# Kernel tuning notes

Measured on AMD Instinct MI355X. Metric: run time of the kernel, lower is better.

The kernel has to match this reference:

```python
import jax, jax.numpy as jnp
import numpy as np

EMBED_DIM = 1024

def setup_inputs() -> dict:
    key = jax.random.key(0)
    k1, k2 = jax.random.split(key)
    x = jax.random.normal(k1, (8, 2048, EMBED_DIM), dtype=jnp.float32)
    # torch nn.Linear weight is [out, in]; emulate default init scale roughly
    W_qkv = jax.random.normal(k2, (3 * EMBED_DIM, EMBED_DIM), dtype=jnp.float32) * (1.0 / np.sqrt(EMBED_DIM))
    b_qkv = jnp.zeros((3 * EMBED_DIM,), dtype=jnp.float32)
    return {"x": x, "W_qkv": W_qkv, "b_qkv": b_qkv}

def reference(x, W_qkv, b_qkv):
    # qkv = x @ W.T + b  -> [B, N, 3E]
    qkv = jnp.einsum('bne,fe->bnf', x, W_qkv) + b_qkv
    q, k, v = jnp.split(qkv, 3, axis=-1)  # each [B, N, E]
    scale = 1.0 / jnp.sqrt(jnp.asarray(EMBED_DIM, dtype=x.dtype))
    scores = jnp.einsum('bqe,bke->bqk', q, k) * scale  # [B, N, N]
    attn = jax.nn.softmax(scores, axis=-1)
    return jnp.einsum('bqk,bke->bqe', attn, v)
```

## Files before the change

kernel.cpp:

```cpp
#include <hip/hip_runtime.h>
#include <hip/hip_bf16.h>

typedef unsigned short u16;
typedef unsigned int   u32;
typedef long long      ll;

#define BATCH   8
#define SEQ     2048
#define EMBED   1024
#define THREE_E 3072

using bf16x8 = __attribute__((ext_vector_type(8))) __bf16;
using f32x4  = __attribute__((ext_vector_type(4))) float;

typedef const __attribute__((address_space(1))) void* as1cv;
typedef __attribute__((address_space(3))) void*       as3v;

__device__ __forceinline__ float bf2f(u16 u) {
  union { float f; u32 i; } c; c.i = ((u32)u) << 16; return c.f;
}
__device__ __forceinline__ u16 f2bf(float f) {
  u32 u = __builtin_bit_cast(u32, f);
  return (u16)((u + 0x7FFFu + ((u >> 16) & 1u)) >> 16);
}

__global__ __launch_bounds__(256) void cast_f32_bf16(const float* __restrict__ in,
                                                     u16* __restrict__ out, int n4) {
  int i = blockIdx.x * 256 + threadIdx.x;
  int stride = gridDim.x * 256;
  for (; i < n4; i += stride) {
    float4 f = ((const float4*)in)[i];
    ushort4 o;
    o.x = f2bf(f.x); o.y = f2bf(f.y); o.z = f2bf(f.z); o.w = f2bf(f.w);
    ((ushort4*)out)[i] = o;
  }
}

template<int STORE_BF16, int HAS_BIAS>
__global__ __launch_bounds__(512) void gemm256(
    const u16* __restrict__ A, const u16* __restrict__ B,
    void* __restrict__ Cv, const float* __restrict__ bias,
    int lda, int ldb, int ldc, int nt, float scale,
    ll sA, ll sB, ll sC, int gx, int gy)
{
  __shared__ __align__(128) char smem[131072];
  const int tid = threadIdx.x;
  const int w  = tid >> 6, l = tid & 63;
  const int lr  = l & 15;
  const int lkb = (l >> 4) * 16;
  const int wm  = w >> 2, wn = w & 3;

  const int nwg = gridDim.x;
  const int id  = blockIdx.x;
  const int sid = (id & 7) * (nwg >> 3) + (id >> 3);
  const int bx  = sid % gx;
  const int tq  = sid / gx;
  const int by  = tq % gy;
  const int bz  = tq / gy;
  const ll  tileM = (ll)by * 256;
  const int tileN = bx * 256;
  A += (ll)bz * sA;
  B += (ll)bz * sB;

  const int rh0  = tid >> 3;
  const int cbyt = ((tid & 7) * 16) ^ ((rh0 & 7) << 4);
  const int kofs = cbyt >> 1;
  const u16* Asrc = A + (tileM + rh0) * lda + kofs;
  const u16* Bsrc = B + ((ll)tileN + (rh0 >> 5) * 64 + (rh0 & 31)) * ldb + kofs;
  char* lwb = smem + w * 1024;

#define STAGE_A(D,H,KT) do{ \
  const u16* g_ = Asrc + (ll)(H)*64*lda + (KT)*64; \
  char* lb_ = lwb + (D)*65536 + (H)*16384; \
  __builtin_amdgcn_global_load_lds((as1cv)g_, (as3v)lb_, 16, 0, 0); \
  __builtin_amdgcn_global_load_lds((as1cv)(g_ + 128LL*lda), (as3v)(lb_ + 8192), 16, 0, 0); \
}while(0)

#define STAGE_B(D,H,KT) do{ \
  const u16* g_ = Bsrc + (ll)(H)*32*ldb + (KT)*64; \
  char* lb_ = lwb + (D)*65536 + 32768 + (H)*16384; \
  __builtin_amdgcn_global_load_lds((as1cv)g_, (as3v)lb_, 16, 0, 0); \
  __builtin_amdgcn_global_load_lds((as1cv)(g_ + 128LL*ldb), (as3v)(lb_ + 8192), 16, 0, 0); \
}while(0)

  bf16x8 a_[4][2], b0_[2][2], b1_[2][2];
  f32x4 acc[8][4] = {};

#define LDA8(D,MH) do{ \
  _Pragma("unroll") for (int mi = 0; mi < 4; ++mi) { \
    const int rh_ = wm*64 + mi*16 + lr; \
    const char* rp_ = smem + (D)*65536 + (MH)*16384 + rh_*128; \
    const int sw_ = (rh_ & 7) << 4; \
    a_[mi][0] = *(const bf16x8*)(rp_ + (lkb ^ sw_)); \
    a_[mi][1] = *(const bf16x8*)(rp_ + ((64 + lkb) ^ sw_)); \
  } \
}while(0)

#define LDB4(BB,D,NH) do{ \
  _Pragma("unroll") for (int ni = 0; ni < 2; ++ni) { \
    const int rh_ = wn*32 + ni*16 + lr; \
    const char* rp_ = smem + (D)*65536 + 32768 + (NH)*16384 + rh_*128; \
    const int sw_ = (rh_ & 7) << 4; \
    BB[ni][0] = *(const bf16x8*)(rp_ + (lkb ^ sw_)); \
    BB[ni][1] = *(const bf16x8*)(rp_ + ((64 + lkb) ^ sw_)); \
  } \
}while(0)

#define MFMA16(MH,NH,BB) do{ \
  __builtin_amdgcn_s_setprio(1); \
  _Pragma("unroll") for (int ks = 0; ks < 2; ++ks) \
    _Pragma("unroll") for (int mi = 0; mi < 4; ++mi) \
      _Pragma("unroll") for (int ni = 0; ni < 2; ++ni) \
        acc[(MH)*4+mi][(NH)*2+ni] = __builtin_amdgcn_mfma_f32_16x16x32_bf16( \
            a_[mi][ks], BB[ni][ks], acc[(MH)*4+mi][(NH)*2+ni], 0, 0, 0); \
  __builtin_amdgcn_s_setprio(0); \
}while(0)

#define BAR() __builtin_amdgcn_s_barrier()
#define WAIT_LGKM0() do{ asm volatile("s_waitcnt lgkmcnt(0)":::"memory"); \
                         __builtin_amdgcn_sched_barrier(0); }while(0)

  STAGE_A(0,0,0); STAGE_B(0,0,0); STAGE_A(0,1,0); STAGE_B(0,1,0);
  STAGE_A(1,0,1); STAGE_B(1,1,1);
  asm volatile("s_waitcnt vmcnt(4)":::"memory");
  BAR();

  const int NI = nt >> 1;
  for (int it = 0; it < NI; ++it) {
    const int k1 = 2*it + 1, k2 = 2*it + 2, k3 = 2*it + 3;
    const bool pf = (it + 1 < NI);
    LDA8(0,0); LDB4(b0_,0,0);
    STAGE_A(1,1,k1);
    asm volatile("s_waitcnt lgkmcnt(8)":::"memory");
    BAR(); WAIT_LGKM0();
    MFMA16(0,0,b0_);
    BAR();
    LDB4(b1_,0,1);
    STAGE_B(1,0,k1);
    BAR(); WAIT_LGKM0();
    MFMA16(0,1,b1_);
    BAR();
    LDA8(0,1);
    if (pf) STAGE_A(0,0,k2);
    BAR(); WAIT_LGKM0();
    MFMA16(1,1,b1_);
    BAR();
    LDB4(b0_,0,0);
    if (pf) STAGE_B(0,1,k2);
    BAR(); WAIT_LGKM0();
    MFMA16(1,0,b0_);
    if (pf) asm volatile("s_waitcnt vmcnt(4)":::"memory");
    else    asm volatile("s_waitcnt vmcnt(0)":::"memory");
    BAR();
    LDA8(1,0); LDB4(b0_,1,0);
    if (pf) STAGE_A(0,1,k2);
    asm volatile("s_waitcnt lgkmcnt(8)":::"memory");
    BAR(); WAIT_LGKM0();
    MFMA16(0,0,b0_);
    BAR();
    LDB4(b1_,1,1);
    if (pf) STAGE_B(0,0,k2);
    BAR(); WAIT_LGKM0();
    MFMA16(0,1,b1_);
    BAR();
    LDA8(1,1);
    if (pf) STAGE_A(1,0,k3);
    BAR(); WAIT_LGKM0();
    MFMA16(1,1,b1_);
    BAR();
    LDB4(b0_,1,0);
    if (pf) STAGE_B(1,1,k3);
    BAR(); WAIT_LGKM0();
    MFMA16(1,0,b0_);
    if (pf) asm volatile("s_waitcnt vmcnt(4)":::"memory");
    else    asm volatile("s_waitcnt vmcnt(0)":::"memory");
    BAR();
  }

  u16*   Cb = (u16*)Cv   + (ll)bz * sC;
  float* Cf = (float*)Cv + (ll)bz * sC;
  const ll rbase = tileM + wm * 128 + (l >> 4) * 4;
#pragma unroll
  for (int m = 0; m < 8; ++m) {
    const ll row0 = rbase + (m >> 2) * 64 + (m & 3) * 16;
#pragma unroll
    for (int n = 0; n < 4; ++n) {
      const int col = tileN + wn * 64 + n * 16 + lr;
      float badd = HAS_BIAS ? bias[col] : 0.0f;
#pragma unroll
      for (int j = 0; j < 4; ++j) {
        float v = acc[m][n][j] * scale + badd;
        if (STORE_BF16) Cb[(row0 + j) * ldc + col] = f2bf(v);
        else            Cf[(row0 + j) * ldc + col] = v;
      }
    }
  }
#undef STAGE_A
#undef STAGE_B
#undef LDA8
#undef LDB4
#undef MFMA16
#undef BAR
#undef WAIT_LGKM0
}

__global__ __launch_bounds__(256) void transpose_v(const u16* __restrict__ qkv,
                                                   u16* __restrict__ Vt) {
  __shared__ u16 tile[64 * 64];
  const int t  = threadIdx.x;
  const int b  = blockIdx.z;
  const int e0 = blockIdx.x * 64;
  const int n0 = blockIdx.y * 64;
  const u16* V  = qkv + (ll)b * SEQ * THREE_E + 2 * EMBED;
  u16* Vtb      = Vt  + (ll)b * EMBED * SEQ;
  const int r = t >> 3;
  const int c = (t & 7) * 8;
#pragma unroll
  for (int p = 0; p < 2; ++p) {
    const int rr = r + p * 32;
    uint4 d = *(const uint4*)&V[(ll)(n0 + rr) * THREE_E + e0 + c];
    *(uint4*)&tile[rr * 64 + (c ^ ((rr & 7) << 3))] = d;
  }
  __syncthreads();
#pragma unroll
  for (int p = 0; p < 2; ++p) {
    const int er = r + p * 32;
    u16 o[8];
#pragma unroll
    for (int i = 0; i < 8; ++i) {
      const int nn = c + i;
      o[i] = tile[nn * 64 + (er ^ ((nn & 7) << 3))];
    }
    *(uint4*)&Vtb[(ll)(e0 + er) * SEQ + n0 + c] = *(const uint4*)o;
  }
}

__global__ __launch_bounds__(256) void softmax_rows(u16* __restrict__ S) {
  const ll row = blockIdx.x;
  u16* p = S + row * SEQ;
  const int t = threadIdx.x;
  uint4 raw = ((const uint4*)p)[t];
  const u16* rs = (const u16*)&raw;
  float v[8];
#pragma unroll
  for (int i = 0; i < 8; ++i) v[i] = bf2f(rs[i]);
  float m = v[0];
#pragma unroll
  for (int i = 1; i < 8; ++i) m = fmaxf(m, v[i]);
#pragma unroll
  for (int off = 32; off > 0; off >>= 1) m = fmaxf(m, __shfl_xor(m, off));
  __shared__ float red[8];
  if ((t & 63) == 0) red[t >> 6] = m;
  __syncthreads();
  m = fmaxf(fmaxf(red[0], red[1]), fmaxf(red[2], red[3]));
  float e[8];
  float s = 0.0f;
#pragma unroll
  for (int i = 0; i < 8; ++i) { e[i] = __expf(v[i] - m); s += e[i]; }
#pragma unroll
  for (int off = 32; off > 0; off >>= 1) s += __shfl_xor(s, off);
  if ((t & 63) == 0) red[4 + (t >> 6)] = s;
  __syncthreads();
  s = red[4] + red[5] + red[6] + red[7];
  const float inv = 1.0f / s;
  u16 o[8];
#pragma unroll
  for (int i = 0; i < 8; ++i) o[i] = f2bf(e[i] * inv);
  ((uint4*)p)[t] = *(const uint4*)o;
}

extern "C" void kernel_launch(void* const* d_in, const int* in_sizes, int n_in,
                              void* d_out, int out_size, void* d_ws, size_t ws_size,
                              hipStream_t stream) {
  const float* x    = (const float*)d_in[0];
  const float* W    = (const float*)d_in[1];
  const float* bias = (const float*)d_in[2];
  float* out = (float*)d_out;
  char* ws = (char*)d_ws;
  (void)in_sizes; (void)n_in; (void)out_size; (void)ws_size;

  u16* qkv = (u16*)ws;
  u16* Sbf = (u16*)(ws + 100663296LL);
  u16* Vt  = (u16*)(ws + 100663296LL + 67108864LL);
  u16* xb  = (u16*)(ws + 100663296LL);
  u16* Wb  = (u16*)(ws + 100663296LL + 33554432LL);

  cast_f32_bf16<<<dim3(2048), dim3(256), 0, stream>>>(x, xb, (BATCH*SEQ*EMBED) / 4);
  cast_f32_bf16<<<dim3(512),  dim3(256), 0, stream>>>(W, Wb, (THREE_E*EMBED) / 4);

  gemm256<1, 1><<<dim3(768), dim3(512), 0, stream>>>(
      xb, Wb, (void*)qkv, bias, EMBED, EMBED, THREE_E, EMBED/64, 1.0f,
      0LL, 0LL, 0LL, 12, 64);

  transpose_v<<<dim3(EMBED/64, SEQ/64, BATCH), dim3(256), 0, stream>>>(qkv, Vt);

  gemm256<1, 0><<<dim3(512), dim3(512), 0, stream>>>(
      qkv, qkv + EMBED, (void*)Sbf, (const float*)nullptr,
      THREE_E, THREE_E, SEQ, EMBED/64, 0.03125f,
      (ll)SEQ * THREE_E, (ll)SEQ * THREE_E, (ll)SEQ * SEQ, 8, 8);

  softmax_rows<<<dim3(BATCH * SEQ), dim3(256), 0, stream>>>(Sbf);

  gemm256<0, 0><<<dim3(256), dim3(512), 0, stream>>>(
      Sbf, Vt, (void*)out, (const float*)nullptr,
      SEQ, SEQ, EMBED, SEQ/64, 1.0f,
      (ll)SEQ * SEQ, (ll)EMBED * SEQ, (ll)SEQ * EMBED, 4, 8);
}
```

Baseline: 388.0 us.

## Restructure GEMM main loop into eight-phase ping-pong with deeper prefetch

Rewrites the bf16 GEMM inner loop as eight uniform phases. Each phase waits on a single combined vmcnt/lgkmcnt barrier, then reads the next LDS fragment, issues a global-to-LDS stage, and runs MFMAs on fragments loaded in the previous phase. It double-buffers the A and B register fragments so LDS reads overlap the MFMAs, and hoists the swizzled LDS pointer math out of the loop. Out-of-range tiles are clamped so loads issue unconditionally rather than behind branches. This adds register pressure and redundant loads near the end of the loop, in exchange for deeper global-load queuing (vmcnt 12).

```diff
diff --git a/kernel.cpp b/kernel.cpp
--- a/kernel.cpp
+++ b/kernel.cpp
@@ -83,98 +83,84 @@
   __builtin_amdgcn_global_load_lds((as1cv)(g_ + 128LL*ldb), (as3v)(lb_ + 8192), 16, 0, 0); \
 }while(0)
 
-  bf16x8 a_[4][2], b0_[2][2], b1_[2][2];
+  const int sw  = (lr & 7) << 4;
+  const int ok0 = lkb ^ sw;
+  const int ok1 = (64 + lkb) ^ sw;
+  const char* pA0k0 = smem + (wm * 64 + lr) * 128 + ok0;
+  const char* pA0k1 = smem + (wm * 64 + lr) * 128 + ok1;
+  const char* pA1k0 = pA0k0 + 65536;
+  const char* pA1k1 = pA0k1 + 65536;
+  const char* pB0k0 = smem + 32768 + (wn * 32 + lr) * 128 + ok0;
+  const char* pB0k1 = smem + 32768 + (wn * 32 + lr) * 128 + ok1;
+  const char* pB1k0 = pB0k0 + 65536;
+  const char* pB1k1 = pB0k1 + 65536;
+
+  bf16x8 aA[4][2], aB[4][2], bX[2][2], bY[2][2];
   f32x4 acc[8][4] = {};
 
-#define LDA8(D,MH) do{ \
+#define READ_A(DST, PK0, PK1, MH) do{ \
   _Pragma("unroll") for (int mi = 0; mi < 4; ++mi) { \
-    const int rh_ = wm*64 + mi*16 + lr; \
-    const char* rp_ = smem + (D)*65536 + (MH)*16384 + rh_*128; \
-    const int sw_ = (rh_ & 7) << 4; \
-    a_[mi][0] = *(const bf16x8*)(rp_ + (lkb ^ sw_)); \
-    a_[mi][1] = *(const bf16x8*)(rp_ + ((64 + lkb) ^ sw_)); \
+    DST[mi][0] = *(const bf16x8*)((PK0) + (MH)*16384 + mi*2048); \
+    DST[mi][1] = *(const bf16x8*)((PK1) + (MH)*16384 + mi*2048); \
   } \
 }while(0)
 
-#define LDB4(BB,D,NH) do{ \
+#define READ_B(DST, PK0, PK1, NH) do{ \
   _Pragma("unroll") for (int ni = 0; ni < 2; ++ni) { \
-    const int rh_ = wn*32 + ni*16 + lr; \
-    const char* rp_ = smem + (D)*65536 + 32768 + (NH)*16384 + rh_*128; \
-    const int sw_ = (rh_ & 7) << 4; \
-    BB[ni][0] = *(const bf16x8*)(rp_ + (lkb ^ sw_)); \
-    BB[ni][1] = *(const bf16x8*)(rp_ + ((64 + lkb) ^ sw_)); \
+    DST[ni][0] = *(const bf16x8*)((PK0) + (NH)*16384 + ni*2048); \
+    DST[ni][1] = *(const bf16x8*)((PK1) + (NH)*16384 + ni*2048); \
   } \
 }while(0)
 
-#define MFMA16(MH,NH,BB) do{ \
+#define MFMA16(MH,NH,AR,BR) do{ \
   __builtin_amdgcn_s_setprio(1); \
   _Pragma("unroll") for (int ks = 0; ks < 2; ++ks) \
     _Pragma("unroll") for (int mi = 0; mi < 4; ++mi) \
       _Pragma("unroll") for (int ni = 0; ni < 2; ++ni) \
         acc[(MH)*4+mi][(NH)*2+ni] = __builtin_amdgcn_mfma_f32_16x16x32_bf16( \
-            a_[mi][ks], BB[ni][ks], acc[(MH)*4+mi][(NH)*2+ni], 0, 0, 0); \
+            AR[mi][ks], BR[ni][ks], acc[(MH)*4+mi][(NH)*2+ni], 0, 0, 0); \
   __builtin_amdgcn_s_setprio(0); \
 }while(0)
 
 #define BAR() __builtin_amdgcn_s_barrier()
-#define WAIT_LGKM0() do{ asm volatile("s_waitcnt lgkmcnt(0)":::"memory"); \
-                         __builtin_amdgcn_sched_barrier(0); }while(0)
-
-  STAGE_A(0,0,0); STAGE_B(0,0,0); STAGE_A(0,1,0); STAGE_B(0,1,0);
-  STAGE_A(1,0,1); STAGE_B(1,1,1);
-  asm volatile("s_waitcnt vmcnt(4)":::"memory");
-  BAR();
+#define SBAR() __builtin_amdgcn_sched_barrier(0)
+#define WAITP() do{ asm volatile("s_waitcnt vmcnt(12) lgkmcnt(0)":::"memory"); \
+                    BAR(); SBAR(); }while(0)
+
+  const int ntm1 = nt - 1;
+
+  STAGE_A(0,0,0); STAGE_B(0,0,0);
+  asm volatile("s_waitcnt vmcnt(0)":::"memory");
+  BAR(); SBAR();
+  READ_A(aA, pA0k0, pA0k1, 0);
+  READ_B(bX, pB0k0, pB0k1, 0);
+  asm volatile("s_waitcnt lgkmcnt(0)":::"memory");
+  BAR(); SBAR();
+  {
+    const int c2p = (2 > ntm1) ? ntm1 : 2;
+    STAGE_B(0,1,0);
+    STAGE_A(0,1,0);
+    STAGE_A(1,0,1);
+    STAGE_B(1,0,1);
+    STAGE_B(1,1,1);
+    STAGE_A(1,1,1);
+    STAGE_A(0,0,c2p);
+  }
 
   const int NI = nt >> 1;
   for (int it = 0; it < NI; ++it) {
-    const int k1 = 2*it + 1, k2 = 2*it + 2, k3 = 2*it + 3;
-    const bool pf = (it + 1 < NI);
-    LDA8(0,0); LDB4(b0_,0,0);
-    STAGE_A(1,1,k1);
-    asm volatile("s_waitcnt lgkmcnt(8)":::"memory");
-    BAR(); WAIT_LGKM0();
-    MFMA16(0,0,b0_);
-    BAR();
-    LDB4(b1_,0,1);
-    STAGE_B(1,0,k1);
-    BAR(); WAIT_LGKM0();
-    MFMA16(0,1,b1_);
-    BAR();
-    LDA8(0,1);
-    if (pf) STAGE_A(0,0,k2);
-    BAR(); WAIT_LGKM0();
-    MFMA16(1,1,b1_);
-    BAR();
-    LDB4(b0_,0,0);
-    if (pf) STAGE_B(0,1,k2);
-    BAR(); WAIT_LGKM0();
-    MFMA16(1,0,b0_);
-    if (pf) asm volatile("s_waitcnt vmcnt(4)":::"memory");
-    else    asm volatile("s_waitcnt vmcnt(0)":::"memory");
-    BAR();
-    LDA8(1,0); LDB4(b0_,1,0);
-    if (pf) STAGE_A(0,1,k2);
-    asm volatile("s_waitcnt lgkmcnt(8)":::"memory");
-    BAR(); WAIT_LGKM0();
-    MFMA16(0,0,b0_);
-    BAR();
-    LDB4(b1_,1,1);
-    if (pf) STAGE_B(0,0,k2);
-    BAR(); WAIT_LGKM0();
-    MFMA16(0,1,b1_);
-    BAR();
-    LDA8(1,1);
-    if (pf) STAGE_A(1,0,k3);
-    BAR(); WAIT_LGKM0();
-    MFMA16(1,1,b1_);
-    BAR();
-    LDB4(b0_,1,0);
-    if (pf) STAGE_B(1,1,k3);
-    BAR(); WAIT_LGKM0();
-    MFMA16(1,0,b0_);
-    if (pf) asm volatile("s_waitcnt vmcnt(4)":::"memory");
-    else    asm volatile("s_waitcnt vmcnt(0)":::"memory");
-    BAR();
+    const int t2 = 2*it + 2, t3 = 2*it + 3, t4 = 2*it + 4;
+    const int c2 = (t2 > ntm1) ? ntm1 : t2;
+    const int c3 = (t3 > ntm1) ? ntm1 : t3;
+    const int c4 = (t4 > ntm1) ? ntm1 : t4;
+    WAITP(); READ_B(bY, pB0k0, pB0k1, 1); STAGE_B(0,0,c2); MFMA16(0,0,aA,bX);
+    WAITP(); READ_A(aB, pA0k0, pA0k1, 1); STAGE_B(0,1,c2); MFMA16(0,1,aA,bY);
+    WAITP(); READ_A(aA, pA1k0, pA1k1, 0); STAGE_A(0,1,c2); MFMA16(1,1,aB,bY);
+    WAITP(); READ_B(bY, pB1k0, pB1k1, 0); STAGE_A(1,0,c3); MFMA16(1,0,aB,bX);
+    WAITP(); READ_B(bX, pB1k0, pB1k1, 1); STAGE_B(1,0,c3); MFMA16(0,0,aA,bY);
+    WAITP(); READ_A(aB, pA1k0, pA1k1, 1); STAGE_B(1,1,c3); MFMA16(0,1,aA,bX);
+    WAITP(); READ_A(aA, pA0k0, pA0k1, 0); STAGE_A(1,1,c3); MFMA16(1,1,aB,bX);
+    WAITP(); READ_B(bX, pB0k0, pB0k1, 0); STAGE_A(0,0,c4); MFMA16(1,0,aB,bY);
   }
 
   u16*   Cb = (u16*)Cv   + (ll)bz * sC;
@@ -197,11 +183,12 @@
   }
 #undef STAGE_A
 #undef STAGE_B
-#undef LDA8
-#undef LDB4
+#undef READ_A
+#undef READ_B
 #undef MFMA16
 #undef BAR
-#undef WAIT_LGKM0
+#undef SBAR
+#undef WAITP
 }
 
 __global__ __launch_bounds__(256) void transpose_v(const u16* __restrict__ qkv,
```

New measurement: 383.7 us. Within noise of the previous version (-1.1%).
